# Optimization experiments

Hardware: AMD Instinct MI355X
Metric: run time of the kernel (lower is better)

The kernel has to match this reference:

```python
import jax, jax.numpy as jnp
import numpy as np

RANK = 16
ALPHA = 16.0
IN_F = 4096
OUT_F = 11008
TOKENS = 64


def setup_inputs() -> dict:
    key = jax.random.key(0)
    k_x, k_w, k_s, k_a, k_b, k_bias = jax.random.split(key, 6)
    return {
        "x": jax.random.normal(k_x, (TOKENS, IN_F), dtype=jnp.float32),
        "weight_int4": jax.random.normal(k_w, (OUT_F, IN_F), dtype=jnp.float32),
        "weight_scale": jax.random.uniform(k_s, (OUT_F,), dtype=jnp.float32),
        "lora_A": jax.random.normal(k_a, (RANK, IN_F), dtype=jnp.float32) * 0.01,
        "lora_B": jax.random.normal(k_b, (OUT_F, RANK), dtype=jnp.float32),
        "bias": jax.random.normal(k_bias, (OUT_F,), dtype=jnp.float32),
    }


def reference(x, weight_int4, weight_scale, lora_A, lora_B, bias):
    # Dequantize: per-output-channel scale.  [out, in]
    weight = weight_int4 * weight_scale[:, None]
    # LoRA delta: B @ A scaled by alpha/rank.  [out, in]
    lora_weight = (lora_B @ lora_A) * (ALPHA / RANK)
    effective_weight = weight + lora_weight
    # F.linear: x @ W^T + b  ->  [tokens, out]
    return x @ effective_weight.T + bias
```

## Files before the change

### kernel.cpp

```cpp
#include <hip/hip_runtime.h>
#include <hip/hip_bf16.h>
#include <cstdint>

#define TOK   64
#define INF   4096
#define OUTF  11008
#define KCHUNKS 128
#define QCNT  8
#define NCHB  172

using bf16x8  = __attribute__((ext_vector_type(8))) __bf16;
using floatx4 = __attribute__((ext_vector_type(4))) float;

union B8u { uint32_t u[4]; uint4 q; bf16x8 v; };

__device__ __forceinline__ uint32_t hi2(float a, float b) {
    return (__float_as_uint(a) >> 16) | (__float_as_uint(b) & 0xffff0000u);
}
__device__ __forceinline__ float losub(float x) {
    return x - __uint_as_float(__float_as_uint(x) & 0xffff0000u);
}
__device__ __forceinline__ void packW(float4 a, float4 b, B8u& wh, B8u& wl) {
    wh.u[0] = hi2(a.x, a.y);  wh.u[1] = hi2(a.z, a.w);
    wh.u[2] = hi2(b.x, b.y);  wh.u[3] = hi2(b.z, b.w);
    wl.u[0] = hi2(losub(a.x), losub(a.y));
    wl.u[1] = hi2(losub(a.z), losub(a.w));
    wl.u[2] = hi2(losub(b.x), losub(b.y));
    wl.u[3] = hi2(losub(b.z), losub(b.w));
}

__global__ __launch_bounds__(256) void k_prep_x(const float* __restrict__ x,
        unsigned short* __restrict__ xh, unsigned short* __restrict__ xl) {
    int idx  = blockIdx.x * 256 + threadIdx.x;
    int j    = idx & 7;
    int lane = (idx >> 3) & 63;
    int kc   = (idx >> 9) & 127;
    int mt   = idx >> 16;
    int row  = mt * 16 + (lane & 15);
    int col  = kc * 32 + ((lane >> 4) << 3) + j;
    float v  = x[(size_t)row * INF + col];
    uint32_t u = __float_as_uint(v);
    float lo = losub(v);
    xh[idx] = (unsigned short)(u >> 16);
    xl[idx] = (unsigned short)(__float_as_uint(lo) >> 16);
}

__global__ __launch_bounds__(256) void k_lora_t(const float* __restrict__ x,
        const float* __restrict__ A, float* __restrict__ tm) {
    int t = blockIdx.x, wv = threadIdx.x >> 6, lane = threadIdx.x & 63;
    int r = blockIdx.y * 4 + wv;
    const float4* xr = (const float4*)(x + (size_t)t * INF);
    const float4* ar = (const float4*)(A + (size_t)r * INF);
    float s = 0.f;
#pragma unroll
    for (int i = 0; i < INF / 4 / 64; ++i) {
        float4 a = xr[lane + i * 64], b = ar[lane + i * 64];
        s += a.x * b.x + a.y * b.y + a.z * b.z + a.w * b.w;
    }
#pragma unroll
    for (int off = 32; off > 0; off >>= 1) s += __shfl_down(s, off);
    if (lane == 0) tm[t * 16 + r] = s;
}

template<bool ATOMIC>
__global__ __launch_bounds__(256, 2) void k_main(const float* __restrict__ W,
        const uint4* __restrict__ xh, const uint4* __restrict__ xl,
        const float* __restrict__ scale, float* __restrict__ part,
        float* __restrict__ out) {
    __shared__ uint4 wlds[2048];
    __shared__ uint4 xsl[2048];

    int tid  = threadIdx.x;
    int lane = tid & 63;
    int wv   = tid >> 6;
    int quad = lane >> 4;
    int nb   = blockIdx.x % NCHB;
    int q    = blockIdx.x / NCHB;
    int chl  = wv * 16 + (lane & 15);
    int ch   = nb * 64 + chl;

    const int kbase = q * 512;
    int rpar = lane >> 5;
    int gg   = lane & 31;

    floatx4 acc[4] = {};

    for (int ph = 0; ph < 4; ++ph) {
        __syncthreads();

#pragma unroll
        for (int t = 0; t < 8; ++t) {
            int i = wv * 8 + t;
            int r = i * 2 + rpar;
            int f = (gg - r) & 31;
            const float* src = W + (size_t)(nb * 64 + r) * INF
                             + kbase + ph * 128 + f * 4;
            __builtin_amdgcn_global_load_lds(
                (const __attribute__((address_space(1))) uint32_t*)src,
                (__attribute__((address_space(3))) uint32_t*)&wlds[i * 64],
                16, 0, 0);
        }
#pragma unroll
        for (int t = 0; t < 8; ++t) {
            int j  = wv * 8 + t;
            int hl = j >> 4, mt = (j >> 2) & 3, kc = j & 3;
            const uint4* src = (hl ? xl : xh)
                + ((size_t)(mt * KCHUNKS + q * 16 + ph * 4 + kc) * 64 + lane);
            __builtin_amdgcn_global_load_lds(
                (const __attribute__((address_space(1))) uint32_t*)src,
                (__attribute__((address_space(3))) uint32_t*)&xsl[j * 64],
                16, 0, 0);
        }
        __syncthreads();

#pragma unroll
        for (int kc = 0; kc < 4; ++kc) {
            int f0 = (kc * 4 + quad) * 2;
            uint4 wf0 = wlds[chl * 32 + ((f0 + chl) & 31)];
            uint4 wf1 = wlds[chl * 32 + ((f0 + 1 + chl) & 31)];
            B8u wh, wl;
            packW(*(float4*)&wf0, *(float4*)&wf1, wh, wl);
#pragma unroll
            for (int mt = 0; mt < 4; ++mt) {
                B8u ah, al;
                ah.q = xsl[(mt * 4 + kc) * 64 + lane];
                al.q = xsl[(16 + mt * 4 + kc) * 64 + lane];
                acc[mt] = __builtin_amdgcn_mfma_f32_16x16x32_bf16(ah.v, wh.v, acc[mt], 0, 0, 0);
                acc[mt] = __builtin_amdgcn_mfma_f32_16x16x32_bf16(ah.v, wl.v, acc[mt], 0, 0, 0);
                acc[mt] = __builtin_amdgcn_mfma_f32_16x16x32_bf16(al.v, wh.v, acc[mt], 0, 0, 0);
            }
        }
    }

#pragma unroll
    for (int mt = 0; mt < 4; ++mt) {
        int token = mt * 16 + quad * 4;
#pragma unroll
        for (int r = 0; r < 4; ++r) {
            if constexpr (ATOMIC) {
                atomicAdd(&out[(size_t)(token + r) * OUTF + ch], scale[ch] * acc[mt][r]);
            } else {
                part[((size_t)q * TOK + token + r) * OUTF + ch] = acc[mt][r];
            }
        }
    }
}

__global__ __launch_bounds__(256) void k_post(const float* __restrict__ part,
        const float* __restrict__ scale, const float* __restrict__ bias,
        const float* __restrict__ lB, const float* __restrict__ tm,
        float* __restrict__ out) {
    int o = blockIdx.x * 256 + threadIdx.x;
    int t = blockIdx.y;
    if (o >= OUTF) return;
    float s = 0.f;
#pragma unroll
    for (int qq = 0; qq < QCNT; ++qq)
        s += part[((size_t)qq * TOK + t) * OUTF + o];
    const float4* Br = (const float4*)(lB + (size_t)o * 16);
    const float4* tr = (const float4*)(tm + (size_t)t * 16);
    float l = 0.f;
#pragma unroll
    for (int i = 0; i < 4; ++i) {
        float4 b = Br[i], tt = tr[i];
        l += b.x * tt.x + b.y * tt.y + b.z * tt.z + b.w * tt.w;
    }
    out[(size_t)t * OUTF + o] = s * scale[o] + l + bias[o];
}

__global__ __launch_bounds__(256) void k_pre(const float* __restrict__ bias,
        const float* __restrict__ lB, const float* __restrict__ tm,
        float* __restrict__ out) {
    int o = blockIdx.x * 256 + threadIdx.x;
    int t = blockIdx.y;
    if (o >= OUTF) return;
    const float4* Br = (const float4*)(lB + (size_t)o * 16);
    const float4* tr = (const float4*)(tm + (size_t)t * 16);
    float l = 0.f;
#pragma unroll
    for (int i = 0; i < 4; ++i) {
        float4 b = Br[i], tt = tr[i];
        l += b.x * tt.x + b.y * tt.y + b.z * tt.z + b.w * tt.w;
    }
    out[(size_t)t * OUTF + o] = l + bias[o];
}

extern "C" void kernel_launch(void* const* d_in, const int* in_sizes, int n_in,
                              void* d_out, int out_size, void* d_ws, size_t ws_size,
                              hipStream_t stream) {
    const float* x     = (const float*)d_in[0];
    const float* W     = (const float*)d_in[1];
    const float* scale = (const float*)d_in[2];
    const float* lA    = (const float*)d_in[3];
    const float* lB    = (const float*)d_in[4];
    const float* bias  = (const float*)d_in[5];
    float* out = (float*)d_out;

    char* ws = (char*)d_ws;
    unsigned short* xh = (unsigned short*)(ws);
    unsigned short* xl = (unsigned short*)(ws + 524288);
    float* tm   = (float*)(ws + 1048576);
    float* part = (float*)(ws + 1052672);
    const size_t need = 1052672 + (size_t)QCNT * TOK * OUTF * 4;

    k_prep_x<<<1024, 256, 0, stream>>>(x, xh, xl);
    k_lora_t<<<dim3(TOK, 4), 256, 0, stream>>>(x, lA, tm);

    if (ws_size >= need) {
        k_main<false><<<NCHB * QCNT, 256, 0, stream>>>(W, (const uint4*)xh,
                (const uint4*)xl, scale, part, out);
        k_post<<<dim3(43, TOK), 256, 0, stream>>>(part, scale, bias, lB, tm, out);
    } else {
        k_pre<<<dim3(43, TOK), 256, 0, stream>>>(bias, lB, tm, out);
        k_main<true><<<NCHB * QCNT, 256, 0, stream>>>(W, (const uint4*)xh,
                (const uint4*)xl, scale, nullptr, out);
    }
}
```

Before: 275.5 us.

## Double-buffer LDS staging in main GEMM and merge prep kernels

The main kernel now splits each K slice into eight smaller phases and uses two LDS buffers. Global-to-LDS loads for the next phase are issued before computing on the current one, so memory traffic overlaps the MFMA work, with one barrier per phase instead of two. The x-split kernel and the LoRA projection kernel are merged into a single launch to save one kernel launch. Total LDS use is unchanged, but there are more, smaller stages, so barrier and address overhead per byte goes up. The kernel is already close to being bound by streaming W from HBM, which caps how much the overlap can help.

Result: no change. 280.8 us (+1.9%).

```diff
diff --git a/kernel.cpp b/kernel.cpp
--- a/kernel.cpp
+++ b/kernel.cpp
@@ -29,37 +29,40 @@
     wl.u[3] = hi2(losub(b.z), losub(b.w));
 }
 
-__global__ __launch_bounds__(256) void k_prep_x(const float* __restrict__ x,
-        unsigned short* __restrict__ xh, unsigned short* __restrict__ xl) {
-    int idx  = blockIdx.x * 256 + threadIdx.x;
-    int j    = idx & 7;
-    int lane = (idx >> 3) & 63;
-    int kc   = (idx >> 9) & 127;
-    int mt   = idx >> 16;
-    int row  = mt * 16 + (lane & 15);
-    int col  = kc * 32 + ((lane >> 4) << 3) + j;
-    float v  = x[(size_t)row * INF + col];
-    uint32_t u = __float_as_uint(v);
-    float lo = losub(v);
-    xh[idx] = (unsigned short)(u >> 16);
-    xl[idx] = (unsigned short)(__float_as_uint(lo) >> 16);
-}
-
-__global__ __launch_bounds__(256) void k_lora_t(const float* __restrict__ x,
-        const float* __restrict__ A, float* __restrict__ tm) {
-    int t = blockIdx.x, wv = threadIdx.x >> 6, lane = threadIdx.x & 63;
-    int r = blockIdx.y * 4 + wv;
-    const float4* xr = (const float4*)(x + (size_t)t * INF);
-    const float4* ar = (const float4*)(A + (size_t)r * INF);
-    float s = 0.f;
-#pragma unroll
-    for (int i = 0; i < INF / 4 / 64; ++i) {
-        float4 a = xr[lane + i * 64], b = ar[lane + i * 64];
-        s += a.x * b.x + a.y * b.y + a.z * b.z + a.w * b.w;
-    }
-#pragma unroll
-    for (int off = 32; off > 0; off >>= 1) s += __shfl_down(s, off);
-    if (lane == 0) tm[t * 16 + r] = s;
+__global__ __launch_bounds__(256) void k_prep(const float* __restrict__ x,
+        const float* __restrict__ A,
+        unsigned short* __restrict__ xh, unsigned short* __restrict__ xl,
+        float* __restrict__ tm) {
+    int b = blockIdx.x;
+    if (b < 1024) {
+        int idx  = b * 256 + threadIdx.x;
+        int j    = idx & 7;
+        int lane = (idx >> 3) & 63;
+        int kc   = (idx >> 9) & 127;
+        int mt   = idx >> 16;
+        int row  = mt * 16 + (lane & 15);
+        int col  = kc * 32 + ((lane >> 4) << 3) + j;
+        float v  = x[(size_t)row * INF + col];
+        float lo = losub(v);
+        xh[idx] = (unsigned short)(__float_as_uint(v) >> 16);
+        xl[idx] = (unsigned short)(__float_as_uint(lo) >> 16);
+    } else {
+        int bb   = b - 1024;
+        int t    = bb & 63;
+        int wv   = threadIdx.x >> 6, lane = threadIdx.x & 63;
+        int r    = (bb >> 6) * 4 + wv;
+        const float4* xr = (const float4*)(x + (size_t)t * INF);
+        const float4* ar = (const float4*)(A + (size_t)r * INF);
+        float s = 0.f;
+#pragma unroll
+        for (int i = 0; i < INF / 4 / 64; ++i) {
+            float4 a = xr[lane + i * 64], c = ar[lane + i * 64];
+            s += a.x * c.x + a.y * c.y + a.z * c.z + a.w * c.w;
+        }
+#pragma unroll
+        for (int off = 32; off > 0; off >>= 1) s += __shfl_down(s, off);
+        if (lane == 0) tm[t * 16 + r] = s;
+    }
 }
 
 template<bool ATOMIC>
@@ -67,8 +70,8 @@
         const uint4* __restrict__ xh, const uint4* __restrict__ xl,
         const float* __restrict__ scale, float* __restrict__ part,
         float* __restrict__ out) {
-    __shared__ uint4 wlds[2048];
-    __shared__ uint4 xsl[2048];
+    __shared__ uint4 wlds[2][1024];
+    __shared__ uint4 xsl [2][1024];
 
     int tid  = threadIdx.x;
     int lane = tid & 63;
@@ -80,56 +83,62 @@
     int ch   = nb * 64 + chl;
 
     const int kbase = q * 512;
-    int rpar = lane >> 5;
-    int gg   = lane & 31;
+    int rr = lane >> 4;
+    int gg = lane & 15;
 
     floatx4 acc[4] = {};
 
-    for (int ph = 0; ph < 4; ++ph) {
-        __syncthreads();
-
-#pragma unroll
-        for (int t = 0; t < 8; ++t) {
-            int i = wv * 8 + t;
-            int r = i * 2 + rpar;
-            int f = (gg - r) & 31;
+    auto stage = [&](int p, int bsel) {
+#pragma unroll
+        for (int t = 0; t < 4; ++t) {
+            int i = wv * 4 + t;
+            int r = i * 4 + rr;
+            int f = (gg - r) & 15;
             const float* src = W + (size_t)(nb * 64 + r) * INF
-                             + kbase + ph * 128 + f * 4;
+                             + kbase + p * 64 + f * 4;
             __builtin_amdgcn_global_load_lds(
                 (const __attribute__((address_space(1))) uint32_t*)src,
-                (__attribute__((address_space(3))) uint32_t*)&wlds[i * 64],
+                (__attribute__((address_space(3))) uint32_t*)&wlds[bsel][i * 64],
                 16, 0, 0);
         }
 #pragma unroll
-        for (int t = 0; t < 8; ++t) {
-            int j  = wv * 8 + t;
-            int hl = j >> 4, mt = (j >> 2) & 3, kc = j & 3;
+        for (int t = 0; t < 4; ++t) {
+            int j  = wv * 4 + t;
+            int hl = j >> 3, mt = (j >> 1) & 3, kc = j & 1;
             const uint4* src = (hl ? xl : xh)
-                + ((size_t)(mt * KCHUNKS + q * 16 + ph * 4 + kc) * 64 + lane);
+                + ((size_t)(mt * KCHUNKS + q * 16 + p * 2 + kc) * 64 + lane);
             __builtin_amdgcn_global_load_lds(
                 (const __attribute__((address_space(1))) uint32_t*)src,
-                (__attribute__((address_space(3))) uint32_t*)&xsl[j * 64],
+                (__attribute__((address_space(3))) uint32_t*)&xsl[bsel][j * 64],
                 16, 0, 0);
         }
+    };
+
+    stage(0, 0);
+    int cur = 0;
+#pragma unroll
+    for (int p = 0; p < 8; ++p) {
         __syncthreads();
-
-#pragma unroll
-        for (int kc = 0; kc < 4; ++kc) {
-            int f0 = (kc * 4 + quad) * 2;
-            uint4 wf0 = wlds[chl * 32 + ((f0 + chl) & 31)];
-            uint4 wf1 = wlds[chl * 32 + ((f0 + 1 + chl) & 31)];
+        if (p < 7) stage(p + 1, cur ^ 1);
+
+#pragma unroll
+        for (int kc = 0; kc < 2; ++kc) {
+            int f0 = kc * 8 + quad * 2;
+            uint4 wf0 = wlds[cur][chl * 16 + ((f0     + chl) & 15)];
+            uint4 wf1 = wlds[cur][chl * 16 + ((f0 + 1 + chl) & 15)];
             B8u wh, wl;
             packW(*(float4*)&wf0, *(float4*)&wf1, wh, wl);
 #pragma unroll
             for (int mt = 0; mt < 4; ++mt) {
                 B8u ah, al;
-                ah.q = xsl[(mt * 4 + kc) * 64 + lane];
-                al.q = xsl[(16 + mt * 4 + kc) * 64 + lane];
+                ah.q = xsl[cur][(    mt * 2 + kc) * 64 + lane];
+                al.q = xsl[cur][(8 + mt * 2 + kc) * 64 + lane];
                 acc[mt] = __builtin_amdgcn_mfma_f32_16x16x32_bf16(ah.v, wh.v, acc[mt], 0, 0, 0);
                 acc[mt] = __builtin_amdgcn_mfma_f32_16x16x32_bf16(ah.v, wl.v, acc[mt], 0, 0, 0);
                 acc[mt] = __builtin_amdgcn_mfma_f32_16x16x32_bf16(al.v, wh.v, acc[mt], 0, 0, 0);
             }
         }
+        cur ^= 1;
     }
 
 #pragma unroll
@@ -203,8 +212,7 @@
     float* part = (float*)(ws + 1052672);
     const size_t need = 1052672 + (size_t)QCNT * TOK * OUTF * 4;
 
-    k_prep_x<<<1024, 256, 0, stream>>>(x, xh, xl);
-    k_lora_t<<<dim3(TOK, 4), 256, 0, stream>>>(x, lA, tm);
+    k_prep<<<1280, 256, 0, stream>>>(x, lA, xh, xl, tm);
 
     if (ws_size >= need) {
         k_main<false><<<NCHB * QCNT, 256, 0, stream>>>(W, (const uint4*)xh,
```
